# Optimization experiments

Hardware: AMD Instinct MI355X
Metric: run time of the kernel (lower is better)

Reference implementation:

```python
import jax, jax.numpy as jnp
import numpy as np

NUM_QUBITS = 12
NUM_LAYERS = 2
STATE_DIM = 2 ** NUM_QUBITS
BATCH = 4096
TWO_PI = 2 * 3.1416  # matches the original initializer constant


def _u3(theta, phi, lam):
    """Single-qubit U3 gate, 2x2 complex64 (matches TF layer exactly)."""
    c = jnp.cos(theta / 2)
    s = jnp.sin(theta / 2)
    z = jnp.zeros_like(phi)
    e_phi = jnp.exp(jax.lax.complex(z, phi))
    e_lam = jnp.exp(jax.lax.complex(z, lam))
    e_pl = jnp.exp(jax.lax.complex(z, phi + lam))
    cc = jax.lax.complex(c, jnp.zeros_like(c))
    sc = jax.lax.complex(s, jnp.zeros_like(s))
    row1 = jnp.stack([cc, -e_lam * sc])
    row2 = jnp.stack([e_phi * sc, e_pl * cc])
    return jnp.stack([row1, row2])  # [2, 2] complex64


def _full_gate(theta_vec, phi_vec, lam_vec):
    """Kronecker product of per-qubit gates -> [2^n, 2^n] complex64."""
    full = _u3(theta_vec[0], phi_vec[0], lam_vec[0])
    for q in range(1, theta_vec.shape[0]):
        full = jnp.kron(full, _u3(theta_vec[q], phi_vec[q], lam_vec[q]))
    return full


def setup_inputs() -> dict:
    key = jax.random.key(0)
    k1, k2, k3, k4 = jax.random.split(key, 4)
    inputs = jax.random.normal(k1, (BATCH, STATE_DIM), dtype=jnp.float32)
    thetas = jax.random.uniform(k2, (NUM_LAYERS, NUM_QUBITS), minval=0.0, maxval=TWO_PI, dtype=jnp.float32)
    phis = jax.random.uniform(k3, (NUM_LAYERS, NUM_QUBITS), minval=0.0, maxval=TWO_PI, dtype=jnp.float32)
    lams = jax.random.uniform(k4, (NUM_LAYERS, NUM_QUBITS), minval=0.0, maxval=TWO_PI, dtype=jnp.float32)
    return {"inputs": inputs, "thetas": thetas, "phis": phis, "lams": lams}


def reference(inputs, thetas, phis, lams):
    # normalize real inputs as complex state, per-sample L2 norm
    state = jax.lax.complex(inputs, jnp.zeros_like(inputs))  # [B, D] complex64
    norm = jnp.linalg.norm(state, axis=1, keepdims=True)      # real, [B, 1]
    state = state / norm
    for l in range(thetas.shape[0]):
        U = _full_gate(thetas[l], phis[l], lams[l])  # [D, D]
        # matvec(U, x) per sample == state @ U^T, batched GEMM replaces tf.map_fn
        state = state @ U.T
    return jnp.real(state * jnp.conj(state))  # probabilities, [B, D] float32
```

## Files before the change

kernel.cpp:

```cpp
#include <hip/hip_runtime.h>
#include <hip/hip_fp16.h>

#define NQ   12
#define DIM  4096
#define NL   2
#define BATCH 4096

typedef float v2f __attribute__((ext_vector_type(2)));


struct PGate { v2f a00, b00, a01, b01, a10, b10, a11, b11; };

__global__ void build_gates(const float* __restrict__ th,
                            const float* __restrict__ ph,
                            const float* __restrict__ lm,
                            float* __restrict__ gates) {
    int q = threadIdx.x;
    if (q >= NQ) return;
    float g00r = 1.f, g00i = 0.f, g01r = 0.f, g01i = 0.f;
    float g10r = 0.f, g10i = 0.f, g11r = 1.f, g11i = 0.f;
    #pragma unroll
    for (int l = 0; l < NL; ++l) {
        float th2 = 0.5f * th[l * NQ + q];
        float p   = ph[l * NQ + q];
        float la  = lm[l * NQ + q];
        float s, c, sl, cl, sp, cp, spl, cpl;
        sincosf(th2, &s, &c);
        sincosf(la, &sl, &cl);
        sincosf(p, &sp, &cp);
        sincosf(p + la, &spl, &cpl);
        float u00r = c,        u00i = 0.f;
        float u01r = -cl * s,  u01i = -sl * s;
        float u10r = cp * s,   u10i = sp * s;
        float u11r = cpl * c,  u11i = spl * c;
        float n00r = u00r*g00r - u00i*g00i + u01r*g10r - u01i*g10i;
        float n00i = u00r*g00i + u00i*g00r + u01r*g10i + u01i*g10r;
        float n01r = u00r*g01r - u00i*g01i + u01r*g11r - u01i*g11i;
        float n01i = u00r*g01i + u00i*g01r + u01r*g11i + u01i*g11r;
        float n10r = u10r*g00r - u10i*g00i + u11r*g10r - u11i*g10i;
        float n10i = u10r*g00i + u10i*g00r + u11r*g10i + u11i*g10r;
        float n11r = u10r*g01r - u10i*g01i + u11r*g11r - u11i*g11i;
        float n11i = u10r*g01i + u10i*g01r + u11r*g11i + u11i*g11r;
        g00r = n00r; g00i = n00i; g01r = n01r; g01i = n01i;
        g10r = n10r; g10i = n10i; g11r = n11r; g11i = n11i;
    }
    int k = (NQ - 1) - q;
    float* o = gates + k * 16;
    o[0]  = g00r;  o[1]  = g00i;  o[2]  = -g00i; o[3]  = g00r;
    o[4]  = g01r;  o[5]  = g01i;  o[6]  = -g01i; o[7]  = g01r;
    o[8]  = g10r;  o[9]  = g10i;  o[10] = -g10i; o[11] = g10r;
    o[12] = g11r;  o[13] = g11i;  o[14] = -g11i; o[15] = g11r;
}

__device__ __forceinline__ v2f blo(v2f x) { return __builtin_shufflevector(x, x, 0, 0); }
__device__ __forceinline__ v2f bhi(v2f x) { return __builtin_shufflevector(x, x, 1, 1); }

__device__ __forceinline__ void papply(v2f v[16], int r0, int r1, const PGate& g) {
    v2f x0 = v[r0], x1 = v[r1];
    v2f x0r = blo(x0), x0i = bhi(x0), x1r = blo(x1), x1i = bhi(x1);
    v[r0] = g.a00 * x0r + g.b00 * x0i + g.a01 * x1r + g.b01 * x1i;
    v[r1] = g.a10 * x0r + g.b10 * x0i + g.a11 * x1r + g.b11 * x1i;
}

__device__ __forceinline__ void papply_rbit(v2f v[16], int rb, const PGate& g) {
    const int m = 1 << rb;
    #pragma unroll
    for (int h = 0; h < 8; ++h) {
        int low = h & (m - 1);
        int r   = ((h & ~(m - 1)) << 1) | low;
        papply(v, r, r | m, g);
    }
}

__device__ __forceinline__ __half2 pack2(v2f x) {
    return __floats2half2_rn(x.x, x.y);
}
__device__ __forceinline__ v2f unpack2(__half2 h) {
    return (v2f){ __low2float(h), __high2float(h) };
}

#define LDS_N 4384

__global__ __launch_bounds__(256, 8)
void qc_sim(const float* __restrict__ in,
            const PGate* __restrict__ gp,
            float* __restrict__ out) {
    __shared__ __half2 st[LDS_N];
    __shared__ float red[4];

    const int t    = threadIdx.x;
    const int lane = t & 63;
    const int b    = blockIdx.x;

    const float4* __restrict__ x4 =
        reinterpret_cast<const float4*>(in + (size_t)b * DIM);
    float4 lA[4];
    #pragma unroll
    for (int j = 0; j < 4; ++j) lA[j] = x4[j * 256 + t];

    float ss = 0.f;
    #pragma unroll
    for (int j = 0; j < 4; ++j)
        ss += lA[j].x*lA[j].x + lA[j].y*lA[j].y + lA[j].z*lA[j].z + lA[j].w*lA[j].w;
    #pragma unroll
    for (int off = 32; off > 0; off >>= 1)
        ss += __shfl_down(ss, off, 64);
    if (lane == 0) red[t >> 6] = ss;

    v2f v[16];

    {
        PGate g0 = gp[0];
        #pragma unroll
        for (int j = 0; j < 4; ++j) {
            v2f x0, x1;
            x0 = (v2f){ lA[j].x, lA[j].x }; x1 = (v2f){ lA[j].y, lA[j].y };
            v[4*j]   = g0.a00 * x0 + g0.a01 * x1;  v[4*j+1] = g0.a10 * x0 + g0.a11 * x1;
            x0 = (v2f){ lA[j].z, lA[j].z }; x1 = (v2f){ lA[j].w, lA[j].w };
            v[4*j+2] = g0.a00 * x0 + g0.a01 * x1;  v[4*j+3] = g0.a10 * x0 + g0.a11 * x1;
        }
        { PGate g = gp[1];  papply_rbit(v, 1, g); }
        { PGate g = gp[10]; papply_rbit(v, 2, g); }
        { PGate g = gp[11]; papply_rbit(v, 3, g); }
    }

    const int A1 = (t << 2) + (t >> 2);
    const int b2 = (t & 3) | (((t >> 2) & 3) << 6)
                 | (((t >> 6) & 3) << 8) | (((t >> 4) & 3) << 10);
    const int A2 = b2 + (b2 >> 4) + 9 * ((t >> 4) & 3);
    const int b3 = (t & 63) | ((t >> 6) << 10);
    const int A3 = b3 + (b3 >> 4) + 9 * (t >> 6);

    #pragma unroll
    for (int r = 0; r < 16; ++r) {
        const int K1 = ((r >> 2) << 10) + ((r >> 2) << 6) + 9 * (r >> 2) + (r & 3);
        st[A1 + K1] = pack2(v[r]);
    }
    #pragma unroll
    for (int r = 0; r < 16; ++r) {
        const int K2 = ((r & 3) << 2) + ((r >> 2) << 4) + (r >> 2);
        v[r] = unpack2(st[A2 + K2]);
    }

    { PGate g = gp[2]; papply_rbit(v, 0, g); }
    { PGate g = gp[3]; papply_rbit(v, 1, g); }
    { PGate g = gp[4]; papply_rbit(v, 2, g); }
    { PGate g = gp[5]; papply_rbit(v, 3, g); }

    #pragma unroll
    for (int r = 0; r < 16; ++r) {
        const int K2 = ((r & 3) << 2) + ((r >> 2) << 4) + (r >> 2);
        st[A2 + K2] = pack2(v[r]);
    }
    __syncthreads();
    #pragma unroll
    for (int r = 0; r < 16; ++r) v[r] = unpack2(st[A3 + 68 * r]);

    { PGate g = gp[6]; papply_rbit(v, 0, g); }
    { PGate g = gp[7]; papply_rbit(v, 1, g); }
    { PGate g = gp[8]; papply_rbit(v, 2, g); }
    { PGate g = gp[9]; papply_rbit(v, 3, g); }

    float inv = 1.0f / (red[0] + red[1] + red[2] + red[3]);
    float* __restrict__ o = out + (size_t)b * DIM;
    #pragma unroll
    for (int r = 0; r < 16; ++r) {
        v2f p2 = v[r] * v[r];
        o[b3 + (r << 6)] = (p2.x + p2.y) * inv;
    }
}

extern "C" void kernel_launch(void* const* d_in, const int* in_sizes, int n_in,
                              void* d_out, int out_size, void* d_ws, size_t ws_size,
                              hipStream_t stream) {
    (void)in_sizes; (void)n_in; (void)out_size; (void)ws_size;
    const float* inputs = (const float*)d_in[0];
    const float* thetas = (const float*)d_in[1];
    const float* phis   = (const float*)d_in[2];
    const float* lams   = (const float*)d_in[3];
    float* gates = (float*)d_ws;
    float* out   = (float*)d_out;

    hipLaunchKernelGGL(build_gates, dim3(1), dim3(64), 0, stream,
                       thetas, phis, lams, gates);
    hipLaunchKernelGGL(qc_sim, dim3(BATCH), dim3(256), 0, stream,
                       inputs, (const PGate*)gates, out);
}
```

Before: 134.2 us.

## Use XOR-swizzled LDS layout, packed RTZ fp16 conversion, and interleaved stores

Replaces the padded LDS transpose layout with an unpadded, XOR-swizzled index scheme that works out from lane bits, with the aim of avoiding bank conflicts. fp16 packing now uses the hardware cvt_pkrtz intrinsic (round-toward-zero) instead of round-to-nearest conversion. The last gate of each stage is fused with the LDS stores so values are written as soon as they are computed. The risks are slightly different rounding and subtle index errors in the new permutations.

```diff
diff --git a/kernel.cpp b/kernel.cpp
--- a/kernel.cpp
+++ b/kernel.cpp
@@ -6,7 +6,8 @@
 #define NL   2
 #define BATCH 4096
 
-typedef float v2f __attribute__((ext_vector_type(2)));
+typedef float  v2f __attribute__((ext_vector_type(2)));
+typedef __fp16 hv2 __attribute__((ext_vector_type(2)));
 
 
 struct PGate { v2f a00, b00, a01, b01, a10, b10, a11, b11; };
@@ -72,20 +73,26 @@
     }
 }
 
-__device__ __forceinline__ __half2 pack2(v2f x) {
-    return __floats2half2_rn(x.x, x.y);
-}
-__device__ __forceinline__ v2f unpack2(__half2 h) {
-    return (v2f){ __low2float(h), __high2float(h) };
-}
-
-#define LDS_N 4384
+__device__ __forceinline__ unsigned packrtz(v2f x) {
+    union { hv2 h; unsigned u; } c;
+    c.h = __builtin_amdgcn_cvt_pkrtz(x.x, x.y);
+    return c.u;
+}
+__device__ __forceinline__ v2f unpackh(unsigned u) {
+    union { unsigned u; hv2 h; } c; c.u = u;
+    return (v2f){ (float)c.h.x, (float)c.h.y };
+}
+
+#define K1W(r) ( (((r)&1)*33) + ((((r)>>1)&1)*66) + ((((r)>>2)&1)*264) + ((((r)>>3)&1)*512) )
+#define K1R(r) (r)
+#define K2W(r) ( ((((r)&1))<<2) | (((((r)>>1)&1))<<3) | (((((r)>>2)&1))<<4) | (((((r)>>3)&1))<<8) )
+#define K3R(r) ( (((r)&1)*36) + ((((r)>>1)&1)*72) + ((((r)>>2)&1)*1024) + ((((r)>>3)&1)*2048) )
 
 __global__ __launch_bounds__(256, 8)
 void qc_sim(const float* __restrict__ in,
             const PGate* __restrict__ gp,
             float* __restrict__ out) {
-    __shared__ __half2 st[LDS_N];
+    __shared__ unsigned st[DIM];
     __shared__ float red[4];
 
     const int t    = threadIdx.x;
@@ -106,6 +113,19 @@
     for (int off = 32; off > 0; off >>= 1)
         ss += __shfl_down(ss, off, 64);
     if (lane == 0) red[t >> 6] = ss;
+
+    const int L0 = lane & 1, L1 = (lane >> 1) & 1, L2 = (lane >> 2) & 1,
+              L3 = (lane >> 3) & 1, L4 = (lane >> 4) & 1, L5 = lane >> 5;
+    const int w  = t >> 6, w0 = w & 1, w1 = w >> 1;
+    const int A1w = L0 | (L1 << 1) | ((L2 ^ L5) << 2) | (L3 << 3) | (L4 << 4)
+                  | (L5 << 7) | (w << 10);
+    const int A1r = L0 | (L1 << 1) | (L3 << 2) | (L4 << 3) | (L2 << 4)
+                  | (L0 << 5) | (L1 << 6) | (L3 << 7) | (L4 << 8) | (L5 << 9)
+                  | (w << 10);
+    const int A2w = L0 | (L1 << 1) | (L2 << 2) | (L3 << 3) | (L4 << 4)
+                  | (L2 << 5) | (L3 << 6) | (L4 << 7) | (L5 << 9) | (w << 10);
+    const int A3  = L0 | (L1 << 1) | (L2 << 2) | (L3 << 3) | ((L4 ^ w0) << 4)
+                  | (w0 << 7) | (L5 << 8) | (w1 << 9);
 
     v2f v[16];
 
@@ -121,40 +141,35 @@
         }
         { PGate g = gp[1];  papply_rbit(v, 1, g); }
         { PGate g = gp[10]; papply_rbit(v, 2, g); }
-        { PGate g = gp[11]; papply_rbit(v, 3, g); }
-    }
-
-    const int A1 = (t << 2) + (t >> 2);
-    const int b2 = (t & 3) | (((t >> 2) & 3) << 6)
-                 | (((t >> 6) & 3) << 8) | (((t >> 4) & 3) << 10);
-    const int A2 = b2 + (b2 >> 4) + 9 * ((t >> 4) & 3);
-    const int b3 = (t & 63) | ((t >> 6) << 10);
-    const int A3 = b3 + (b3 >> 4) + 9 * (t >> 6);
-
-    #pragma unroll
-    for (int r = 0; r < 16; ++r) {
-        const int K1 = ((r >> 2) << 10) + ((r >> 2) << 6) + 9 * (r >> 2) + (r & 3);
-        st[A1 + K1] = pack2(v[r]);
-    }
-    #pragma unroll
-    for (int r = 0; r < 16; ++r) {
-        const int K2 = ((r & 3) << 2) + ((r >> 2) << 4) + (r >> 2);
-        v[r] = unpack2(st[A2 + K2]);
-    }
+        { PGate g = gp[11];
+          #pragma unroll
+          for (int h = 0; h < 8; ++h) {
+              papply(v, h, h | 8, g);
+              st[A1w ^ K1W(h)]     = packrtz(v[h]);
+              st[A1w ^ K1W(h | 8)] = packrtz(v[h | 8]);
+          }
+        }
+    }
+
+    #pragma unroll
+    for (int r = 0; r < 16; ++r) v[r] = unpackh(st[A1r ^ K1R(r)]);
 
     { PGate g = gp[2]; papply_rbit(v, 0, g); }
     { PGate g = gp[3]; papply_rbit(v, 1, g); }
     { PGate g = gp[4]; papply_rbit(v, 2, g); }
-    { PGate g = gp[5]; papply_rbit(v, 3, g); }
-
-    #pragma unroll
-    for (int r = 0; r < 16; ++r) {
-        const int K2 = ((r & 3) << 2) + ((r >> 2) << 4) + (r >> 2);
-        st[A2 + K2] = pack2(v[r]);
-    }
+    { PGate g = gp[5];
+      #pragma unroll
+      for (int h = 0; h < 8; ++h) {
+          papply(v, h, h | 8, g);
+          st[A2w ^ K2W(h)]     = packrtz(v[h]);
+          st[A2w ^ K2W(h | 8)] = packrtz(v[h | 8]);
+      }
+    }
+
     __syncthreads();
-    #pragma unroll
-    for (int r = 0; r < 16; ++r) v[r] = unpack2(st[A3 + 68 * r]);
+
+    #pragma unroll
+    for (int r = 0; r < 16; ++r) v[r] = unpackh(st[A3 ^ K3R(r)]);
 
     { PGate g = gp[6]; papply_rbit(v, 0, g); }
     { PGate g = gp[7]; papply_rbit(v, 1, g); }
@@ -162,11 +177,12 @@
     { PGate g = gp[9]; papply_rbit(v, 3, g); }
 
     float inv = 1.0f / (red[0] + red[1] + red[2] + red[3]);
+    const int sbase = lane | (w << 10);
     float* __restrict__ o = out + (size_t)b * DIM;
     #pragma unroll
     for (int r = 0; r < 16; ++r) {
         v2f p2 = v[r] * v[r];
-        o[b3 + (r << 6)] = (p2.x + p2.y) * inv;
+        o[sbase + (r << 6)] = (p2.x + p2.y) * inv;
     }
 }
 
```

Result: no change. 132.4 us (-1.4%).

## Apply fused gates as two 64x64 Kronecker-factor MFMA matmuls per sample

Applied to the files above, without the earlier changes.

The per-qubit butterfly updates are replaced by splitting the 12-qubit operator into two 6-qubit Kronecker factors. Each factor is built as a 64x64 complex matrix in fp16 MFMA fragment layout by the setup kernel. Each sample's state is treated as a 64x64 matrix and multiplied on both sides with 32x32x16 f16 MFMA instructions, using swizzled LDS staging in between. This trades scalar FMA work for matrix cores, at the cost of a heavier setup kernel, more registers, lower occupancy (launch bounds 2) and fp16 round-toward-zero conversions of activations.

```diff
diff --git a/kernel.cpp b/kernel.cpp
--- a/kernel.cpp
+++ b/kernel.cpp
@@ -6,167 +6,196 @@
 #define NL   2
 #define BATCH 4096
 
-typedef float v2f __attribute__((ext_vector_type(2)));
-
-
-struct PGate { v2f a00, b00, a01, b01, a10, b10, a11, b11; };
+typedef _Float16 half8  __attribute__((ext_vector_type(8)));
+typedef float    f32x16 __attribute__((ext_vector_type(16)));
+typedef __fp16   hv2    __attribute__((ext_vector_type(2)));
+
+
+union U4H8 { uint4 u; half8 h; };
+
+__device__ __forceinline__ unsigned pkrtz(float a, float b) {
+    union { hv2 h; unsigned u; } c;
+    c.h = __builtin_amdgcn_cvt_pkrtz(a, b);
+    return c.u;
+}
 
 __global__ void build_gates(const float* __restrict__ th,
                             const float* __restrict__ ph,
                             const float* __restrict__ lm,
-                            float* __restrict__ gates) {
-    int q = threadIdx.x;
-    if (q >= NQ) return;
-    float g00r = 1.f, g00i = 0.f, g01r = 0.f, g01i = 0.f;
-    float g10r = 0.f, g10i = 0.f, g11r = 1.f, g11i = 0.f;
-    #pragma unroll
-    for (int l = 0; l < NL; ++l) {
-        float th2 = 0.5f * th[l * NQ + q];
-        float p   = ph[l * NQ + q];
-        float la  = lm[l * NQ + q];
-        float s, c, sl, cl, sp, cp, spl, cpl;
-        sincosf(th2, &s, &c);
-        sincosf(la, &sl, &cl);
-        sincosf(p, &sp, &cp);
-        sincosf(p + la, &spl, &cpl);
-        float u00r = c,        u00i = 0.f;
-        float u01r = -cl * s,  u01i = -sl * s;
-        float u10r = cp * s,   u10i = sp * s;
-        float u11r = cpl * c,  u11i = spl * c;
-        float n00r = u00r*g00r - u00i*g00i + u01r*g10r - u01i*g10i;
-        float n00i = u00r*g00i + u00i*g00r + u01r*g10i + u01i*g10r;
-        float n01r = u00r*g01r - u00i*g01i + u01r*g11r - u01i*g11i;
-        float n01i = u00r*g01i + u00i*g01r + u01r*g11i + u01i*g11r;
-        float n10r = u10r*g00r - u10i*g00i + u11r*g10r - u11i*g10i;
-        float n10i = u10r*g00i + u10i*g00r + u11r*g10i + u11i*g10r;
-        float n11r = u10r*g01r - u10i*g01i + u11r*g11r - u11i*g11i;
-        float n11i = u10r*g01i + u10i*g01r + u11r*g11i + u11i*g11r;
-        g00r = n00r; g00i = n00i; g01r = n01r; g01i = n01i;
-        g10r = n10r; g10i = n10i; g11r = n11r; g11i = n11i;
-    }
-    int k = (NQ - 1) - q;
-    float* o = gates + k * 16;
-    o[0]  = g00r;  o[1]  = g00i;  o[2]  = -g00i; o[3]  = g00r;
-    o[4]  = g01r;  o[5]  = g01i;  o[6]  = -g01i; o[7]  = g01r;
-    o[8]  = g10r;  o[9]  = g10i;  o[10] = -g10i; o[11] = g10r;
-    o[12] = g11r;  o[13] = g11i;  o[14] = -g11i; o[15] = g11r;
-}
-
-__device__ __forceinline__ v2f blo(v2f x) { return __builtin_shufflevector(x, x, 0, 0); }
-__device__ __forceinline__ v2f bhi(v2f x) { return __builtin_shufflevector(x, x, 1, 1); }
-
-__device__ __forceinline__ void papply(v2f v[16], int r0, int r1, const PGate& g) {
-    v2f x0 = v[r0], x1 = v[r1];
-    v2f x0r = blo(x0), x0i = bhi(x0), x1r = blo(x1), x1i = bhi(x1);
-    v[r0] = g.a00 * x0r + g.b00 * x0i + g.a01 * x1r + g.b01 * x1i;
-    v[r1] = g.a10 * x0r + g.b10 * x0i + g.a11 * x1r + g.b11 * x1i;
-}
-
-__device__ __forceinline__ void papply_rbit(v2f v[16], int rb, const PGate& g) {
-    const int m = 1 << rb;
-    #pragma unroll
-    for (int h = 0; h < 8; ++h) {
-        int low = h & (m - 1);
-        int r   = ((h & ~(m - 1)) << 1) | low;
-        papply(v, r, r | m, g);
-    }
-}
-
-__device__ __forceinline__ __half2 pack2(v2f x) {
-    return __floats2half2_rn(x.x, x.y);
-}
-__device__ __forceinline__ v2f unpack2(__half2 h) {
-    return (v2f){ __low2float(h), __high2float(h) };
-}
-
-#define LDS_N 4384
-
-__global__ __launch_bounds__(256, 8)
+                            unsigned short* __restrict__ ws) {
+    __shared__ float g[12][8];
+    int t = threadIdx.x;
+    if (t < NQ) {
+        int q = t;
+        float g00r = 1.f, g00i = 0.f, g01r = 0.f, g01i = 0.f;
+        float g10r = 0.f, g10i = 0.f, g11r = 1.f, g11i = 0.f;
+        #pragma unroll
+        for (int l = 0; l < NL; ++l) {
+            float th2 = 0.5f * th[l * NQ + q];
+            float p   = ph[l * NQ + q];
+            float la  = lm[l * NQ + q];
+            float s, c, sl, cl, sp, cp, spl, cpl;
+            sincosf(th2, &s, &c);
+            sincosf(la, &sl, &cl);
+            sincosf(p, &sp, &cp);
+            sincosf(p + la, &spl, &cpl);
+            float u00r = c,        u00i = 0.f;
+            float u01r = -cl * s,  u01i = -sl * s;
+            float u10r = cp * s,   u10i = sp * s;
+            float u11r = cpl * c,  u11i = spl * c;
+            float n00r = u00r*g00r - u00i*g00i + u01r*g10r - u01i*g10i;
+            float n00i = u00r*g00i + u00i*g00r + u01r*g10i + u01i*g10r;
+            float n01r = u00r*g01r - u00i*g01i + u01r*g11r - u01i*g11i;
+            float n01i = u00r*g01i + u00i*g01r + u01r*g11i + u01i*g11r;
+            float n10r = u10r*g00r - u10i*g00i + u11r*g10r - u11i*g10i;
+            float n10i = u10r*g00i + u10i*g00r + u11r*g10i + u11i*g10r;
+            float n11r = u10r*g01r - u10i*g01i + u11r*g11r - u11i*g11i;
+            float n11i = u10r*g01i + u10i*g01r + u11r*g11i + u11i*g11r;
+            g00r = n00r; g00i = n00i; g01r = n01r; g01i = n01i;
+            g10r = n10r; g10i = n10i; g11r = n11r; g11i = n11i;
+        }
+        g[q][0] = g00r; g[q][1] = g00i; g[q][2] = g01r; g[q][3] = g01i;
+        g[q][4] = g10r; g[q][5] = g10i; g[q][6] = g11r; g[q][7] = g11i;
+    }
+    __syncthreads();
+
+    for (int idx = t; idx < 24576; idx += 256) {
+        int arr  = idx >> 13;
+        int rem  = idx & 8191;
+        int frag = rem >> 9;
+        int lane = (rem >> 3) & 63;
+        int j    = rem & 7;
+        int row, col, base, k, nn = 0;
+        if (arr == 0) {
+            int n4 = frag >> 2, ks = frag & 3;
+            nn  = n4 * 32 + (lane & 31);
+            k   = ks * 16 + ((lane >> 5) << 3) + j;
+            row = nn & 63; col = k; base = 6;
+        } else {
+            int m = frag >> 3, ks = frag & 7;
+            row = m * 32 + (lane & 31);
+            k   = ks * 16 + ((lane >> 5) << 3) + j;
+            col = k & 63; base = 0;
+        }
+        float re = 1.f, im = 0.f;
+        #pragma unroll
+        for (int qq = 0; qq < 6; ++qq) {
+            const float* G = g[base + qq];
+            int rb = (row >> (5 - qq)) & 1;
+            int cb = (col >> (5 - qq)) & 1;
+            float fr = G[rb * 4 + cb * 2], fi = G[rb * 4 + cb * 2 + 1];
+            float nre = re * fr - im * fi;
+            float nim = re * fi + im * fr;
+            re = nre; im = nim;
+        }
+        float val;
+        if (arr == 0)      val = (nn < 64) ? re : im;
+        else if (arr == 1) val = (k < 64) ? re : -im;
+        else               val = (k < 64) ? im :  re;
+        union { __fp16 h; unsigned short s; } cv;
+        cv.h = (__fp16)val;
+        ws[idx] = cv.s;
+    }
+}
+
+__global__ __launch_bounds__(256, 2)
 void qc_sim(const float* __restrict__ in,
-            const PGate* __restrict__ gp,
+            const unsigned short* __restrict__ gw,
             float* __restrict__ out) {
-    __shared__ __half2 st[LDS_N];
+    __shared__ unsigned Xh32[2048];
+    __shared__ unsigned Tc32[4096];
     __shared__ float red[4];
 
-    const int t    = threadIdx.x;
-    const int lane = t & 63;
-    const int b    = blockIdx.x;
+    const int t = threadIdx.x, lane = t & 63, w = t >> 6, b = blockIdx.x;
+    const int m1 = w & 1, ng = (w >> 1) * 2;
+    const int m2 = w & 1, n2 = w >> 1;
+
+    const uint4* __restrict__ wsv = reinterpret_cast<const uint4*>(gw);
+    uint4 g1b[2][4], m1f[8], m2f[8];
+    #pragma unroll
+    for (int n = 0; n < 2; ++n)
+        #pragma unroll
+        for (int ks = 0; ks < 4; ++ks)
+            g1b[n][ks] = wsv[((ng + n) * 4 + ks) * 64 + lane];
+    #pragma unroll
+    for (int ks = 0; ks < 8; ++ks) m1f[ks] = wsv[1024 + (m2 * 8 + ks) * 64 + lane];
+    #pragma unroll
+    for (int ks = 0; ks < 8; ++ks) m2f[ks] = wsv[2048 + (m2 * 8 + ks) * 64 + lane];
 
     const float4* __restrict__ x4 =
         reinterpret_cast<const float4*>(in + (size_t)b * DIM);
-    float4 lA[4];
-    #pragma unroll
-    for (int j = 0; j < 4; ++j) lA[j] = x4[j * 256 + t];
+    float4 lX[4];
+    #pragma unroll
+    for (int j = 0; j < 4; ++j) lX[j] = x4[j * 256 + t];
 
     float ss = 0.f;
     #pragma unroll
     for (int j = 0; j < 4; ++j)
-        ss += lA[j].x*lA[j].x + lA[j].y*lA[j].y + lA[j].z*lA[j].z + lA[j].w*lA[j].w;
-    #pragma unroll
-    for (int off = 32; off > 0; off >>= 1)
-        ss += __shfl_down(ss, off, 64);
-    if (lane == 0) red[t >> 6] = ss;
-
-    v2f v[16];
-
-    {
-        PGate g0 = gp[0];
-        #pragma unroll
-        for (int j = 0; j < 4; ++j) {
-            v2f x0, x1;
-            x0 = (v2f){ lA[j].x, lA[j].x }; x1 = (v2f){ lA[j].y, lA[j].y };
-            v[4*j]   = g0.a00 * x0 + g0.a01 * x1;  v[4*j+1] = g0.a10 * x0 + g0.a11 * x1;
-            x0 = (v2f){ lA[j].z, lA[j].z }; x1 = (v2f){ lA[j].w, lA[j].w };
-            v[4*j+2] = g0.a00 * x0 + g0.a01 * x1;  v[4*j+3] = g0.a10 * x0 + g0.a11 * x1;
-        }
-        { PGate g = gp[1];  papply_rbit(v, 1, g); }
-        { PGate g = gp[10]; papply_rbit(v, 2, g); }
-        { PGate g = gp[11]; papply_rbit(v, 3, g); }
-    }
-
-    const int A1 = (t << 2) + (t >> 2);
-    const int b2 = (t & 3) | (((t >> 2) & 3) << 6)
-                 | (((t >> 6) & 3) << 8) | (((t >> 4) & 3) << 10);
-    const int A2 = b2 + (b2 >> 4) + 9 * ((t >> 4) & 3);
-    const int b3 = (t & 63) | ((t >> 6) << 10);
-    const int A3 = b3 + (b3 >> 4) + 9 * (t >> 6);
-
+        ss += lX[j].x*lX[j].x + lX[j].y*lX[j].y + lX[j].z*lX[j].z + lX[j].w*lX[j].w;
+    #pragma unroll
+    for (int off = 32; off > 0; off >>= 1) ss += __shfl_down(ss, off, 64);
+    if (lane == 0) red[w] = ss;
+
+    #pragma unroll
+    for (int j = 0; j < 4; ++j) {
+        int fi = (j * 256 + t) * 4, r = fi >> 6, c = fi & 63;
+        int a32 = r * 32 + ((((c >> 3) ^ (r & 7)) << 2)) + ((c & 7) >> 1);
+        Xh32[a32]     = pkrtz(lX[j].x, lX[j].y);
+        Xh32[a32 + 1] = pkrtz(lX[j].z, lX[j].w);
+    }
+    __syncthreads();
+    const float inv = 1.0f / (red[0] + red[1] + red[2] + red[3]);
+
+    f32x16 acc0 = {0,0,0,0,0,0,0,0,0,0,0,0,0,0,0,0};
+    f32x16 acc1 = {0,0,0,0,0,0,0,0,0,0,0,0,0,0,0,0};
+    const int rowX = m1 * 32 + (lane & 31);
+    #pragma unroll
+    for (int ks = 0; ks < 4; ++ks) {
+        int kb  = ks * 16 + ((lane >> 5) << 3);
+        int a32 = rowX * 32 + ((((kb >> 3) ^ (rowX & 7)) << 2));
+        U4H8 xf; xf.u = *reinterpret_cast<const uint4*>(&Xh32[a32]);
+        U4H8 b0; b0.u = g1b[0][ks];
+        U4H8 b1; b1.u = g1b[1][ks];
+        acc0 = __builtin_amdgcn_mfma_f32_32x32x16_f16(xf.h, b0.h, acc0, 0, 0, 0);
+        acc1 = __builtin_amdgcn_mfma_f32_32x32x16_f16(xf.h, b1.h, acc1, 0, 0, 0);
+    }
+
+    #pragma unroll
+    for (int tile = 0; tile < 2; ++tile) {
+        int nt = ng + tile;
+        const f32x16& acc = tile ? acc1 : acc0;
+        int kofs = m1 * 32 + 64 * (nt >> 1) + ((lane >> 5) << 2);
+        int cc   = (nt & 1) * 32 + (lane & 31);
+        #pragma unroll
+        for (int p = 0; p < 4; ++p) {
+            int k0  = kofs + p * 8;
+            int a32 = cc * 64 + (((k0 >> 3) ^ (cc & 15)) << 2) + ((k0 & 7) >> 1);
+            Tc32[a32]     = pkrtz(acc[4 * p],     acc[4 * p + 1]);
+            Tc32[a32 + 1] = pkrtz(acc[4 * p + 2], acc[4 * p + 3]);
+        }
+    }
+    __syncthreads();
+
+    f32x16 accR = {0,0,0,0,0,0,0,0,0,0,0,0,0,0,0,0};
+    f32x16 accI = {0,0,0,0,0,0,0,0,0,0,0,0,0,0,0,0};
+    const int cT = n2 * 32 + (lane & 31);
+    #pragma unroll
+    for (int ks = 0; ks < 8; ++ks) {
+        int kb  = ks * 16 + ((lane >> 5) << 3);
+        int a32 = cT * 64 + (((kb >> 3) ^ (cT & 15)) << 2);
+        U4H8 tf; tf.u = *reinterpret_cast<const uint4*>(&Tc32[a32]);
+        U4H8 a1; a1.u = m1f[ks];
+        U4H8 a2; a2.u = m2f[ks];
+        accR = __builtin_amdgcn_mfma_f32_32x32x16_f16(a1.h, tf.h, accR, 0, 0, 0);
+        accI = __builtin_amdgcn_mfma_f32_32x32x16_f16(a2.h, tf.h, accI, 0, 0, 0);
+    }
+
+    float* __restrict__ o = out + (size_t)b * DIM
+        + (size_t)((m2 * 32 + ((lane >> 5) << 2)) * 64 + n2 * 32 + (lane & 31));
     #pragma unroll
     for (int r = 0; r < 16; ++r) {
-        const int K1 = ((r >> 2) << 10) + ((r >> 2) << 6) + 9 * (r >> 2) + (r & 3);
-        st[A1 + K1] = pack2(v[r]);
-    }
-    #pragma unroll
-    for (int r = 0; r < 16; ++r) {
-        const int K2 = ((r & 3) << 2) + ((r >> 2) << 4) + (r >> 2);
-        v[r] = unpack2(st[A2 + K2]);
-    }
-
-    { PGate g = gp[2]; papply_rbit(v, 0, g); }
-    { PGate g = gp[3]; papply_rbit(v, 1, g); }
-    { PGate g = gp[4]; papply_rbit(v, 2, g); }
-    { PGate g = gp[5]; papply_rbit(v, 3, g); }
-
-    #pragma unroll
-    for (int r = 0; r < 16; ++r) {
-        const int K2 = ((r & 3) << 2) + ((r >> 2) << 4) + (r >> 2);
-        st[A2 + K2] = pack2(v[r]);
-    }
-    __syncthreads();
-    #pragma unroll
-    for (int r = 0; r < 16; ++r) v[r] = unpack2(st[A3 + 68 * r]);
-
-    { PGate g = gp[6]; papply_rbit(v, 0, g); }
-    { PGate g = gp[7]; papply_rbit(v, 1, g); }
-    { PGate g = gp[8]; papply_rbit(v, 2, g); }
-    { PGate g = gp[9]; papply_rbit(v, 3, g); }
-
-    float inv = 1.0f / (red[0] + red[1] + red[2] + red[3]);
-    float* __restrict__ o = out + (size_t)b * DIM;
-    #pragma unroll
-    for (int r = 0; r < 16; ++r) {
-        v2f p2 = v[r] * v[r];
-        o[b3 + (r << 6)] = (p2.x + p2.y) * inv;
+        int off = ((r & 3) + 8 * (r >> 2)) * 64;
+        o[off] = (accR[r] * accR[r] + accI[r] * accI[r]) * inv;
     }
 }
 
@@ -178,11 +207,11 @@
     const float* thetas = (const float*)d_in[1];
     const float* phis   = (const float*)d_in[2];
     const float* lams   = (const float*)d_in[3];
-    float* gates = (float*)d_ws;
-    float* out   = (float*)d_out;
-
-    hipLaunchKernelGGL(build_gates, dim3(1), dim3(64), 0, stream,
+    unsigned short* gates = (unsigned short*)d_ws;
+    float* out = (float*)d_out;
+
+    hipLaunchKernelGGL(build_gates, dim3(1), dim3(256), 0, stream,
                        thetas, phis, lams, gates);
     hipLaunchKernelGGL(qc_sim, dim3(BATCH), dim3(256), 0, stream,
-                       inputs, (const PGate*)gates, out);
-}
+                       inputs, gates, out);
+}
```

Measured after the change: 137.8 us. +2.7%, slower.
